# Kernel tuning notes

Hardware: AMD Instinct MI355X
Metric: run time of the kernel (lower is better)

Reference implementation:

```python
import jax, jax.numpy as jnp
import numpy as np

N = 1048576
HID = 64
GEO = 15


def _glorot(key, in_dim, out_dim):
    # torch nn.Linear default init: U(-1/sqrt(in), 1/sqrt(in)); stored here as [in, out]
    bound = 1.0 / np.sqrt(in_dim)
    return jax.random.uniform(key, (in_dim, out_dim), jnp.float32, -bound, bound)


def setup_inputs() -> dict:
    key = jax.random.key(0)
    ks = jax.random.split(key, 8)
    x = jax.random.normal(ks[0], (N, 6), dtype=jnp.float32)
    # sigma_net: 3 -> 64 -> 64 -> (1 + geo_feat_dim)=16, no bias
    ws0 = _glorot(ks[1], 3, HID)
    ws1 = _glorot(ks[2], HID, HID)
    ws2 = _glorot(ks[3], HID, 1 + GEO)
    # color_net: (3 + 15)=18 -> 64 -> 64 -> 3, no bias
    wc0 = _glorot(ks[4], 3 + GEO, HID)
    wc1 = _glorot(ks[5], HID, HID)
    wc2 = _glorot(ks[6], HID, HID)
    wc3 = _glorot(ks[7], HID, 3)
    return {"x": x, "ws0": ws0, "ws1": ws1, "ws2": ws2,
            "wc0": wc0, "wc1": wc1, "wc2": wc2, "wc3": wc3}


def reference(x, ws0, ws1, ws2, wc0, wc1, wc2, wc3):
    input_pts, input_views = x[..., :3], x[..., 3:]
    # sigma net: Linear+ReLU x2, final Linear
    h = jax.nn.relu(input_pts @ ws0)
    h = jax.nn.relu(h @ ws1)
    h = h @ ws2                       # [N, 16]
    sigma = jax.nn.softplus(h[..., 0])  # [N]
    geo_feat = h[..., 1:]               # [N, 15]
    # color net
    c = jnp.concatenate([input_views, geo_feat], axis=-1)  # [N, 18]
    c = jax.nn.relu(c @ wc0)
    c = jax.nn.relu(c @ wc1)
    c = jax.nn.relu(c @ wc2)
    color = c @ wc3                    # [N, 3]
    return jnp.concatenate([color, sigma[..., None]], axis=-1)  # [N, 4]
```

## Files before the change

kernel.cpp:

```cpp
#include <hip/hip_runtime.h>
#include <math.h>
#include <stdint.h>

typedef short bf16x8 __attribute__((ext_vector_type(8)));
typedef float f32x4 __attribute__((ext_vector_type(4)));

#define NFRAGS 36
#define T 2
#define NW 4
#define BS 256
#define PTS_BLK (NW * T * 16)

__device__ __forceinline__ uint32_t f2bf_rne(float f) {
    uint32_t u = __float_as_uint(f);
    return (u + 0x7FFFu + ((u >> 16) & 1u)) >> 16;
}

__device__ __forceinline__ uint32_t pk2(float a, float b) {
    return __builtin_amdgcn_perm(__float_as_uint(b), __float_as_uint(a), 0x07060302u);
}
__device__ __forceinline__ uint32_t relu2(uint32_t x) {
    uint32_t r;
    asm("v_pk_max_i16 %0, %1, 0" : "=v"(r) : "v"(x));
    return r;
}
__device__ __forceinline__ uint32_t pk2r(float a, float b) {
    return relu2(pk2(a, b));
}
__device__ __forceinline__ uint16_t bfu(float v) {
    return (uint16_t)(__float_as_uint(v) >> 16);
}
__device__ __forceinline__ int sperm(int k) {
    return (k & 3) | (((k >> 2) & 3) << 4) | (((k >> 4) & 3) << 2);
}

__global__ void pack_weights(const float* __restrict__ ws0, const float* __restrict__ ws1,
                             const float* __restrict__ ws2, const float* __restrict__ wc0,
                             const float* __restrict__ wc1, const float* __restrict__ wc2,
                             const float* __restrict__ wc3, uint4* __restrict__ wpack) {
    int idx = blockIdx.x * blockDim.x + threadIdx.x;
    if (idx >= NFRAGS * 64) return;
    int F = idx >> 6, cl = idx & 63, cm = cl & 15, cq = cl >> 4;
    const float* w; int IN, OUT, mt, ks, pm;
    if (F < 4)       { w = ws0; IN = 3;  OUT = 64; mt = F;            ks = 0;          pm = 0; }
    else if (F < 12) { w = ws1; IN = 64; OUT = 64; mt = (F-4) >> 1;   ks = (F-4) & 1;  pm = 1; }
    else if (F < 14) { w = ws2; IN = 64; OUT = 16; mt = 0;            ks = F - 12;     pm = 1; }
    else if (F < 18) { w = wc0; IN = 18; OUT = 64; mt = F - 14;       ks = 0;          pm = 0; }
    else if (F < 26) { w = wc1; IN = 64; OUT = 64; mt = (F-18) >> 1;  ks = (F-18) & 1; pm = 1; }
    else if (F < 34) { w = wc2; IN = 64; OUT = 64; mt = (F-26) >> 1;  ks = (F-26) & 1; pm = 1; }
    else             { w = wc3; IN = 64; OUT = 3;  mt = 0;            ks = F - 34;     pm = 1; }
    const int fo = mt * 16 + cm;
    uint32_t pk[4];
    for (int jj = 0; jj < 4; ++jj) {
        uint32_t h[2];
        for (int bb = 0; bb < 2; ++bb) {
            int kg = ks * 32 + cq * 8 + jj * 2 + bb;
            int kr = pm ? sperm(kg) : kg;
            float v = 0.f;
            if (fo < OUT && kr < IN) v = w[kr * OUT + fo];
            h[bb] = f2bf_rne(v);
        }
        pk[jj] = h[0] | (h[1] << 16);
    }
    wpack[F * 64 + cl] = make_uint4(pk[0], pk[1], pk[2], pk[3]);
}

__global__ __launch_bounds__(BS, 4) void nerf_main(const float* __restrict__ xin,
                                                   const uint4* __restrict__ wpack,
                                                   float* __restrict__ outp, int n) {
    __shared__ __align__(16) char smem[NW * T * 2048];
    const int tid = threadIdx.x, wv = tid >> 6, lane = tid & 63;
    const int p = lane & 15, q = lane >> 4;
    const int sw = p & 7;
    char* actw = smem + wv * (T * 2048);
    const int base = blockIdx.x * PTS_BLK + wv * (T * 16);

    auto aaddr = [&](int t, int g) -> char* {
        return actw + t * 2048 + p * 128 + ((g ^ sw) << 4);
    };

    auto ldA = [&](int F) -> bf16x8 {
        uint4 u = wpack[F * 64 + lane];
        return *(bf16x8*)&u;
    };
    const f32x4 z4 = {0.f, 0.f, 0.f, 0.f};

    float vv0 = 0.f, vv1 = 0.f, vv2 = 0.f;
    {
        float x0 = 0.f, x1 = 0.f, x2 = 0.f;
        const int pi = base + q * 16 + p;
        if (q < T && pi < n) {
            const float2* xp = (const float2*)(xin + (size_t)pi * 6);
            float2 a = xp[0], b = xp[1], c = xp[2];
            x0 = a.x; x1 = a.y; x2 = b.x; vv0 = b.y; vv1 = c.x; vv2 = c.y;
        }
        if (q < T) {
            *(uint4*)aaddr(q, 0) = make_uint4(pk2(x0, x1), pk2(x2, 0.f), 0u, 0u);
            *(uint4*)aaddr(q, 1) = make_uint4(0u, 0u, 0u, 0u);
            *(uint4*)aaddr(q, 2) = make_uint4(0u, 0u, 0u, 0u);
            *(uint4*)aaddr(q, 3) = make_uint4(0u, 0u, 0u, 0u);
        }
    }

    auto storeD = [&](int t, const f32x4* d) {
        *(uint4*)aaddr(t, 2*q)   = make_uint4(pk2r(d[0][0], d[0][1]), pk2r(d[0][2], d[0][3]),
                                              pk2r(d[1][0], d[1][1]), pk2r(d[1][2], d[1][3]));
        *(uint4*)aaddr(t, 2*q+1) = make_uint4(pk2r(d[2][0], d[2][1]), pk2r(d[2][2], d[2][3]),
                                              pk2r(d[3][0], d[3][1]), pk2r(d[3][2], d[3][3]));
    };

    {
        bf16x8 A0 = ldA(0), A1 = ldA(1), A2 = ldA(2), A3 = ldA(3);
        bf16x8 b[T];
#pragma unroll
        for (int t = 0; t < T; ++t) b[t] = *(const bf16x8*)aaddr(t, q);
        f32x4 d[T][4];
#pragma unroll
        for (int t = 0; t < T; ++t) {
            d[t][0] = __builtin_amdgcn_mfma_f32_16x16x32_bf16(A0, b[t], z4, 0, 0, 0);
            d[t][1] = __builtin_amdgcn_mfma_f32_16x16x32_bf16(A1, b[t], z4, 0, 0, 0);
            d[t][2] = __builtin_amdgcn_mfma_f32_16x16x32_bf16(A2, b[t], z4, 0, 0, 0);
            d[t][3] = __builtin_amdgcn_mfma_f32_16x16x32_bf16(A3, b[t], z4, 0, 0, 0);
        }
#pragma unroll
        for (int t = 0; t < T; ++t) storeD(t, d[t]);
    }

    auto layer64 = [&](int FB) {
        bf16x8 A[8];
#pragma unroll
        for (int i = 0; i < 8; ++i) A[i] = ldA(FB + i);
        bf16x8 b0[T], b1[T];
#pragma unroll
        for (int t = 0; t < T; ++t) {
            b0[t] = *(const bf16x8*)aaddr(t, q);
            b1[t] = *(const bf16x8*)aaddr(t, 4 + q);
        }
        f32x4 d[T][4];
#pragma unroll
        for (int t = 0; t < T; ++t) {
#pragma unroll
            for (int mt = 0; mt < 4; ++mt) {
                f32x4 acc = __builtin_amdgcn_mfma_f32_16x16x32_bf16(A[mt*2],   b0[t], z4,  0, 0, 0);
                d[t][mt]  = __builtin_amdgcn_mfma_f32_16x16x32_bf16(A[mt*2+1], b1[t], acc, 0, 0, 0);
            }
        }
#pragma unroll
        for (int t = 0; t < T; ++t) storeD(t, d[t]);
    };

    layer64(4);

    float sig[T];
    {
        bf16x8 A0 = ldA(12), A1 = ldA(13);
        bf16x8 b0[T], b1[T];
#pragma unroll
        for (int t = 0; t < T; ++t) {
            b0[t] = *(const bf16x8*)aaddr(t, q);
            b1[t] = *(const bf16x8*)aaddr(t, 4 + q);
        }
        f32x4 d[T];
#pragma unroll
        for (int t = 0; t < T; ++t) {
            f32x4 acc = __builtin_amdgcn_mfma_f32_16x16x32_bf16(A0, b0[t], z4,  0, 0, 0);
            d[t]      = __builtin_amdgcn_mfma_f32_16x16x32_bf16(A1, b1[t], acc, 0, 0, 0);
        }
#pragma unroll
        for (int t = 0; t < T; ++t) {
            const float sx = d[t][0];
            sig[t] = fmaxf(sx, 0.f) + __logf(1.f + __expf(-fabsf(sx)));
            *(uint4*)aaddr(t, q) = make_uint4(0u, 0u, 0u, 0u);
            if (q == t) {
                *(uint32_t*)(aaddr(t, 0) + 0) = pk2(vv0, vv1);
                *(uint16_t*)(aaddr(t, 0) + 4) = bfu(vv2);
            }
            if (q == 0) {
                *(uint16_t*)(aaddr(t, 0) + 6) = bfu(d[t][1]);
                *(uint32_t*)(aaddr(t, 0) + 8) = pk2(d[t][2], d[t][3]);
            } else if (q == 1) {
                *(uint32_t*)(aaddr(t, 0) + 12) = pk2(d[t][0], d[t][1]);
                *(uint32_t*)(aaddr(t, 1) + 0)  = pk2(d[t][2], d[t][3]);
            } else if (q == 2) {
                *(uint32_t*)(aaddr(t, 1) + 4) = pk2(d[t][0], d[t][1]);
                *(uint32_t*)(aaddr(t, 1) + 8) = pk2(d[t][2], d[t][3]);
            } else {
                *(uint32_t*)(aaddr(t, 1) + 12) = pk2(d[t][0], d[t][1]);
                *(uint32_t*)(aaddr(t, 2) + 0)  = pk2(d[t][2], d[t][3]);
            }
        }
    }

    {
        bf16x8 A0 = ldA(14), A1 = ldA(15), A2 = ldA(16), A3 = ldA(17);
        bf16x8 b[T];
#pragma unroll
        for (int t = 0; t < T; ++t) b[t] = *(const bf16x8*)aaddr(t, q);
        f32x4 d[T][4];
#pragma unroll
        for (int t = 0; t < T; ++t) {
            d[t][0] = __builtin_amdgcn_mfma_f32_16x16x32_bf16(A0, b[t], z4, 0, 0, 0);
            d[t][1] = __builtin_amdgcn_mfma_f32_16x16x32_bf16(A1, b[t], z4, 0, 0, 0);
            d[t][2] = __builtin_amdgcn_mfma_f32_16x16x32_bf16(A2, b[t], z4, 0, 0, 0);
            d[t][3] = __builtin_amdgcn_mfma_f32_16x16x32_bf16(A3, b[t], z4, 0, 0, 0);
        }
#pragma unroll
        for (int t = 0; t < T; ++t) storeD(t, d[t]);
    }

    layer64(18);
    layer64(26);

    {
        bf16x8 A0 = ldA(34), A1 = ldA(35);
        bf16x8 b0[T], b1[T];
#pragma unroll
        for (int t = 0; t < T; ++t) {
            b0[t] = *(const bf16x8*)aaddr(t, q);
            b1[t] = *(const bf16x8*)aaddr(t, 4 + q);
        }
#pragma unroll
        for (int t = 0; t < T; ++t) {
            f32x4 acc = __builtin_amdgcn_mfma_f32_16x16x32_bf16(A0, b0[t], z4,  0, 0, 0);
            f32x4 d   = __builtin_amdgcn_mfma_f32_16x16x32_bf16(A1, b1[t], acc, 0, 0, 0);
            if (q == 0) {
                const int pt = base + t * 16 + p;
                if (pt < n)
                    *(float4*)(outp + (size_t)pt * 4) = make_float4(d[0], d[1], d[2], sig[t]);
            }
        }
    }
}

extern "C" void kernel_launch(void* const* d_in, const int* in_sizes, int n_in,
                              void* d_out, int out_size, void* d_ws, size_t ws_size,
                              hipStream_t stream) {
    const float* x   = (const float*)d_in[0];
    const float* ws0 = (const float*)d_in[1];
    const float* ws1 = (const float*)d_in[2];
    const float* ws2 = (const float*)d_in[3];
    const float* wc0 = (const float*)d_in[4];
    const float* wc1 = (const float*)d_in[5];
    const float* wc2 = (const float*)d_in[6];
    const float* wc3 = (const float*)d_in[7];
    float* out = (float*)d_out;
    uint4* wpack = (uint4*)d_ws;

    const int n = in_sizes[0] / 6;
    pack_weights<<<(NFRAGS * 64 + 255) / 256, 256, 0, stream>>>(ws0, ws1, ws2, wc0, wc1, wc2, wc3, wpack);
    const int grid = (n + PTS_BLK - 1) / PTS_BLK;
    nerf_main<<<grid, BS, 0, stream>>>(x, wpack, out, n);
}
```

Before: 123.6 us.

## Keep activations in registers via permlane32 swap instead of LDS round-trip

Replaces the LDS store/load of each hidden layer's output with an in-register transpose built on v_permlane32_swap. The weight packing gains an extra K-permutation (rperm) so the swapped register layout matches the MFMA B-operand layout. This removes LDS writes, reads and their waits between the 64-wide layers. In exchange, more VGPRs stay live across layers, which could reduce occupancy.

```diff
diff --git a/kernel.cpp b/kernel.cpp
--- a/kernel.cpp
+++ b/kernel.cpp
@@ -24,14 +24,14 @@
     asm("v_pk_max_i16 %0, %1, 0" : "=v"(r) : "v"(x));
     return r;
 }
-__device__ __forceinline__ uint32_t pk2r(float a, float b) {
-    return relu2(pk2(a, b));
-}
-__device__ __forceinline__ uint16_t bfu(float v) {
-    return (uint16_t)(__float_as_uint(v) >> 16);
-}
+__device__ __forceinline__ uint32_t pk2r(float a, float b) { return relu2(pk2(a, b)); }
+__device__ __forceinline__ uint16_t bfu(float v) { return (uint16_t)(__float_as_uint(v) >> 16); }
+
 __device__ __forceinline__ int sperm(int k) {
     return (k & 3) | (((k >> 2) & 3) << 4) | (((k >> 4) & 3) << 2);
+}
+__device__ __forceinline__ int rperm(int k) {
+    return (k & 32) | (((k >> 3) & 1) << 4) | (((k >> 4) & 1) << 3) | (k & 7);
 }
 
 __global__ void pack_weights(const float* __restrict__ ws0, const float* __restrict__ ws1,
@@ -43,19 +43,19 @@
     int F = idx >> 6, cl = idx & 63, cm = cl & 15, cq = cl >> 4;
     const float* w; int IN, OUT, mt, ks, pm;
     if (F < 4)       { w = ws0; IN = 3;  OUT = 64; mt = F;            ks = 0;          pm = 0; }
-    else if (F < 12) { w = ws1; IN = 64; OUT = 64; mt = (F-4) >> 1;   ks = (F-4) & 1;  pm = 1; }
-    else if (F < 14) { w = ws2; IN = 64; OUT = 16; mt = 0;            ks = F - 12;     pm = 1; }
+    else if (F < 12) { w = ws1; IN = 64; OUT = 64; mt = (F-4) >> 1;   ks = (F-4) & 1;  pm = 2; }
+    else if (F < 14) { w = ws2; IN = 64; OUT = 16; mt = 0;            ks = F - 12;     pm = 2; }
     else if (F < 18) { w = wc0; IN = 18; OUT = 64; mt = F - 14;       ks = 0;          pm = 0; }
-    else if (F < 26) { w = wc1; IN = 64; OUT = 64; mt = (F-18) >> 1;  ks = (F-18) & 1; pm = 1; }
-    else if (F < 34) { w = wc2; IN = 64; OUT = 64; mt = (F-26) >> 1;  ks = (F-26) & 1; pm = 1; }
-    else             { w = wc3; IN = 64; OUT = 3;  mt = 0;            ks = F - 34;     pm = 1; }
+    else if (F < 26) { w = wc1; IN = 64; OUT = 64; mt = (F-18) >> 1;  ks = (F-18) & 1; pm = 2; }
+    else if (F < 34) { w = wc2; IN = 64; OUT = 64; mt = (F-26) >> 1;  ks = (F-26) & 1; pm = 2; }
+    else             { w = wc3; IN = 64; OUT = 3;  mt = 0;            ks = F - 34;     pm = 2; }
     const int fo = mt * 16 + cm;
     uint32_t pk[4];
     for (int jj = 0; jj < 4; ++jj) {
         uint32_t h[2];
         for (int bb = 0; bb < 2; ++bb) {
             int kg = ks * 32 + cq * 8 + jj * 2 + bb;
-            int kr = pm ? sperm(kg) : kg;
+            int kr = (pm == 2) ? sperm(rperm(kg)) : kg;
             float v = 0.f;
             if (fo < OUT && kr < IN) v = w[kr * OUT + fo];
             h[bb] = f2bf_rne(v);
@@ -78,12 +78,24 @@
     auto aaddr = [&](int t, int g) -> char* {
         return actw + t * 2048 + p * 128 + ((g ^ sw) << 4);
     };
-
     auto ldA = [&](int F) -> bf16x8 {
         uint4 u = wpack[F * 64 + lane];
         return *(bf16x8*)&u;
     };
     const f32x4 z4 = {0.f, 0.f, 0.f, 0.f};
+
+    auto xpose = [&](const f32x4* d, bf16x8& b0, bf16x8& b1) {
+        uint32_t X0 = pk2r(d[0][0], d[0][1]), X1 = pk2r(d[0][2], d[0][3]);
+        uint32_t X2 = pk2r(d[1][0], d[1][1]), X3 = pk2r(d[1][2], d[1][3]);
+        uint32_t X4 = pk2r(d[2][0], d[2][1]), X5 = pk2r(d[2][2], d[2][3]);
+        uint32_t X6 = pk2r(d[3][0], d[3][1]), X7 = pk2r(d[3][2], d[3][3]);
+        asm("v_permlane32_swap_b32 %0, %1" : "+v"(X0), "+v"(X4));
+        asm("v_permlane32_swap_b32 %0, %1" : "+v"(X1), "+v"(X5));
+        asm("v_permlane32_swap_b32 %0, %1" : "+v"(X2), "+v"(X6));
+        asm("v_permlane32_swap_b32 %0, %1" : "+v"(X3), "+v"(X7));
+        uint4 u0 = make_uint4(X0, X1, X2, X3), u1 = make_uint4(X4, X5, X6, X7);
+        b0 = *(bf16x8*)&u0; b1 = *(bf16x8*)&u1;
+    };
 
     float vv0 = 0.f, vv1 = 0.f, vv2 = 0.f;
     {
@@ -102,12 +114,7 @@
         }
     }
 
-    auto storeD = [&](int t, const f32x4* d) {
-        *(uint4*)aaddr(t, 2*q)   = make_uint4(pk2r(d[0][0], d[0][1]), pk2r(d[0][2], d[0][3]),
-                                              pk2r(d[1][0], d[1][1]), pk2r(d[1][2], d[1][3]));
-        *(uint4*)aaddr(t, 2*q+1) = make_uint4(pk2r(d[2][0], d[2][1]), pk2r(d[2][2], d[2][3]),
-                                              pk2r(d[3][0], d[3][1]), pk2r(d[3][2], d[3][3]));
-    };
+    bf16x8 c0[T], c1[T];
 
     {
         bf16x8 A0 = ldA(0), A1 = ldA(1), A2 = ldA(2), A3 = ldA(3);
@@ -123,30 +130,24 @@
             d[t][3] = __builtin_amdgcn_mfma_f32_16x16x32_bf16(A3, b[t], z4, 0, 0, 0);
         }
 #pragma unroll
-        for (int t = 0; t < T; ++t) storeD(t, d[t]);
+        for (int t = 0; t < T; ++t) xpose(d[t], c0[t], c1[t]);
     }
 
     auto layer64 = [&](int FB) {
         bf16x8 A[8];
 #pragma unroll
         for (int i = 0; i < 8; ++i) A[i] = ldA(FB + i);
-        bf16x8 b0[T], b1[T];
-#pragma unroll
-        for (int t = 0; t < T; ++t) {
-            b0[t] = *(const bf16x8*)aaddr(t, q);
-            b1[t] = *(const bf16x8*)aaddr(t, 4 + q);
-        }
         f32x4 d[T][4];
 #pragma unroll
         for (int t = 0; t < T; ++t) {
 #pragma unroll
             for (int mt = 0; mt < 4; ++mt) {
-                f32x4 acc = __builtin_amdgcn_mfma_f32_16x16x32_bf16(A[mt*2],   b0[t], z4,  0, 0, 0);
-                d[t][mt]  = __builtin_amdgcn_mfma_f32_16x16x32_bf16(A[mt*2+1], b1[t], acc, 0, 0, 0);
-            }
-        }
-#pragma unroll
-        for (int t = 0; t < T; ++t) storeD(t, d[t]);
+                f32x4 acc = __builtin_amdgcn_mfma_f32_16x16x32_bf16(A[mt*2],   c0[t], z4,  0, 0, 0);
+                d[t][mt]  = __builtin_amdgcn_mfma_f32_16x16x32_bf16(A[mt*2+1], c1[t], acc, 0, 0, 0);
+            }
+        }
+#pragma unroll
+        for (int t = 0; t < T; ++t) xpose(d[t], c0[t], c1[t]);
     };
 
     layer64(4);
@@ -154,17 +155,11 @@
     float sig[T];
     {
         bf16x8 A0 = ldA(12), A1 = ldA(13);
-        bf16x8 b0[T], b1[T];
-#pragma unroll
-        for (int t = 0; t < T; ++t) {
-            b0[t] = *(const bf16x8*)aaddr(t, q);
-            b1[t] = *(const bf16x8*)aaddr(t, 4 + q);
-        }
         f32x4 d[T];
 #pragma unroll
         for (int t = 0; t < T; ++t) {
-            f32x4 acc = __builtin_amdgcn_mfma_f32_16x16x32_bf16(A0, b0[t], z4,  0, 0, 0);
-            d[t]      = __builtin_amdgcn_mfma_f32_16x16x32_bf16(A1, b1[t], acc, 0, 0, 0);
+            f32x4 acc = __builtin_amdgcn_mfma_f32_16x16x32_bf16(A0, c0[t], z4,  0, 0, 0);
+            d[t]      = __builtin_amdgcn_mfma_f32_16x16x32_bf16(A1, c1[t], acc, 0, 0, 0);
         }
 #pragma unroll
         for (int t = 0; t < T; ++t) {
@@ -205,7 +200,7 @@
             d[t][3] = __builtin_amdgcn_mfma_f32_16x16x32_bf16(A3, b[t], z4, 0, 0, 0);
         }
 #pragma unroll
-        for (int t = 0; t < T; ++t) storeD(t, d[t]);
+        for (int t = 0; t < T; ++t) xpose(d[t], c0[t], c1[t]);
     }
 
     layer64(18);
@@ -213,16 +208,10 @@
 
     {
         bf16x8 A0 = ldA(34), A1 = ldA(35);
-        bf16x8 b0[T], b1[T];
-#pragma unroll
-        for (int t = 0; t < T; ++t) {
-            b0[t] = *(const bf16x8*)aaddr(t, q);
-            b1[t] = *(const bf16x8*)aaddr(t, 4 + q);
-        }
-#pragma unroll
-        for (int t = 0; t < T; ++t) {
-            f32x4 acc = __builtin_amdgcn_mfma_f32_16x16x32_bf16(A0, b0[t], z4,  0, 0, 0);
-            f32x4 d   = __builtin_amdgcn_mfma_f32_16x16x32_bf16(A1, b1[t], acc, 0, 0, 0);
+#pragma unroll
+        for (int t = 0; t < T; ++t) {
+            f32x4 acc = __builtin_amdgcn_mfma_f32_16x16x32_bf16(A0, c0[t], z4,  0, 0, 0);
+            f32x4 d   = __builtin_amdgcn_mfma_f32_16x16x32_bf16(A1, c1[t], acc, 0, 0, 0);
             if (q == 0) {
                 const int pt = base + t * 16 + p;
                 if (pt < n)
```

Result: no change. 122.8 us (-0.6%).
